# Kernel tuning notes

Measured on AMD Instinct MI355X. Metric: run time of the kernel, lower is better.

The kernel has to match this reference:

```python
import jax, jax.numpy as jnp
import numpy as np

D = 1024      # model dim
DH = 64       # dim_head
H = 8         # heads
INNER = DH * H
L = 6         # depth
NL = 64       # num_latents
MF = 128      # max_num_frames
FF = 4 * D    # ff_mult * dim
B, T, F, V = 4, 8, 4, 256


def _ln(x, g, b):
    m = x.mean(-1, keepdims=True)
    v = x.var(-1, keepdims=True)
    return (x - m) / jnp.sqrt(v + 1e-5) * g + b


def setup_inputs() -> dict:
    key = jax.random.key(0)
    ks = jax.random.split(key, 8)
    s = 0.02
    x = jax.random.normal(ks[0], (B, T, F, V, D), jnp.float32)
    latents = jax.random.normal(ks[1], (NL, D), jnp.float32)
    frame_embs = jax.random.normal(ks[2], (MF, D), jnp.float32)
    Wq = jax.random.normal(ks[3], (L, D, INNER), jnp.float32) * s
    Wkv = jax.random.normal(ks[4], (L, D, 2 * INNER), jnp.float32) * s
    Wo = jax.random.normal(ks[5], (L, INNER, D), jnp.float32) * s
    W1 = jax.random.normal(ks[6], (L, D, FF), jnp.float32) * s
    W2 = jax.random.normal(ks[7], (L, FF, D), jnp.float32) * s
    ones = jnp.ones((L, D), jnp.float32)
    zeros = jnp.zeros((L, D), jnp.float32)
    return dict(
        x=x, latents=latents, frame_embs=frame_embs,
        g_media=ones, b_media=zeros, g_lat=ones, b_lat=zeros,
        Wq=Wq, Wkv=Wkv, Wo=Wo, g_ff=ones, b_ff=zeros, W1=W1, W2=W2,
        g_out=jnp.ones((D,), jnp.float32), b_out=jnp.zeros((D,), jnp.float32),
    )


def reference(x, latents, frame_embs, g_media, b_media, g_lat, b_lat,
              Wq, Wkv, Wo, g_ff, b_ff, W1, W2, g_out, b_out):
    scale = DH ** -0.5
    # add frame embeddings (indexed by T, as in original code), merge F,v dims
    x = x + frame_embs[:T][None, :, None, None, :]
    x = x.reshape(B, T, F * V, D)
    lat0 = jnp.broadcast_to(latents, (B, T, NL, D))

    def split_heads(a):  # (b, t, n, h*d) -> (b, h, t, n, d)
        return a.reshape(B, T, -1, H, DH).transpose(0, 3, 1, 2, 4)

    def block(lat, p):
        gm, bm, gl, bl, wq, wkv, wo, gf, bf, w1, w2 = p
        xm = _ln(x, gm, bm)
        ln_l = _ln(lat, gl, bl)
        q = (ln_l @ wq) * scale
        kv = jnp.concatenate([xm, ln_l], axis=-2) @ wkv
        k, v = jnp.split(kv, 2, axis=-1)
        q, k, v = split_heads(q), split_heads(k), split_heads(v)
        sim = jnp.einsum('bhtid,bhtjd->bhtij', q, k)
        attn = jax.nn.softmax(sim, axis=-1)
        o = jnp.einsum('bhtij,bhtjd->bhtid', attn, v)
        o = o.transpose(0, 2, 3, 1, 4).reshape(B, T, NL, INNER)
        lat = o @ wo + lat
        ff = jax.nn.gelu(_ln(lat, gf, bf) @ w1, approximate=False) @ w2
        return lat + ff, None

    lat, _ = jax.lax.scan(block, lat0,
                          (g_media, b_media, g_lat, b_lat, Wq, Wkv, Wo,
                           g_ff, b_ff, W1, W2))
    return _ln(lat, g_out, b_out)
```

## Files before the change

### kernel.cpp

```cpp
#include <hip/hip_runtime.h>
#include <math.h>

#define D_      1024
#define DH_     64
#define H_      8
#define INNER_  512
#define L_      6
#define NL_     64
#define FF_     4096
#define B_      4
#define T_      8
#define FV_     1024
#define BT_     32
#define MROWS_  32768
#define NKV_    1088
#define KVROWS_ 34816
#define ZB_     256

typedef __bf16 bf16;
typedef __bf16 bf16x8 __attribute__((ext_vector_type(8)));
typedef __bf16 bf16x4 __attribute__((ext_vector_type(4)));
typedef float  f32x4  __attribute__((ext_vector_type(4)));

#define BARRIER() { asm volatile("" ::: "memory"); __builtin_amdgcn_s_barrier(); asm volatile("" ::: "memory"); }
// ... 47 lines not shown
                                                 float* __restrict__ lat) {
    int row = blockIdx.x;
    int i = row & 63;
    int c = threadIdx.x * 4;
    float4 v = *(const float4*)(latents + (size_t)i * D_ + c);
    *(float4*)(lat + (size_t)row * D_ + c) = v;
}

template<int OUTF>
__global__ __launch_bounds__(256) void ln_k(const float* __restrict__ in,
                                            const float* __restrict__ g,
                                            const float* __restrict__ b,
                                            void* __restrict__ out) {
    __shared__ float red[8];
    int row = blockIdx.x;
    const float* x = in + (size_t)row * D_;
    int tid = threadIdx.x, c = tid * 4;
    float4 v = *(const float4*)(x + c);
    float s = v.x + v.y + v.z + v.w;
    float ss = v.x * v.x + v.y * v.y + v.z * v.z + v.w * v.w;
    s = wred_sum(s); ss = wred_sum(ss);
    if ((tid & 63) == 0) { red[tid >> 6] = s; red[4 + (tid >> 6)] = ss; }
    __syncthreads();
    s = red[0] + red[1] + red[2] + red[3];
    ss = red[4] + red[5] + red[6] + red[7];
    float mean = s * (1.0f / D_);
    float rstd = rsqrtf(ss * (1.0f / D_) - mean * mean + 1e-5f);
    float4 gv = *(const float4*)(g + c);
    float4 bv = *(const float4*)(b + c);
    float o0 = (v.x - mean) * rstd * gv.x + bv.x;
    float o1 = (v.y - mean) * rstd * gv.y + bv.y;
    float o2 = (v.z - mean) * rstd * gv.z + bv.z;
    float o3 = (v.w - mean) * rstd * gv.w + bv.w;
    if (OUTF) {
        *(float4*)((float*)out + (size_t)row * D_ + c) = make_float4(o0, o1, o2, o3);
    } else {
        bf16x4 o; o[0] = (bf16)o0; o[1] = (bf16)o1; o[2] = (bf16)o2; o[3] = (bf16)o3;
        *(bf16x4*)((bf16*)out + (size_t)row * D_ + c) = o;
    }
}

template<int NP, int OUTF>
__global__ __launch_bounds__(256) void accln_k(float* __restrict__ lat,
                                               const float* __restrict__ p, long long s,
                                               const float* __restrict__ g,
                                               const float* __restrict__ b,
                                               void* __restrict__ out) {
    __shared__ float red[8];
    int row = blockIdx.x;
    int tid = threadIdx.x, c = tid * 4;
    float* lr = lat + (size_t)row * D_;
    float4 a = *(const float4*)(lr + c);
#pragma unroll
    for (int w = 0; w < NP; w++) {
        float4 x = *(const float4*)(p + (size_t)w * s + (size_t)row * D_ + c);
        a.x += x.x; a.y += x.y; a.z += x.z; a.w += x.w;
    }
    if (!OUTF) *(float4*)(lr + c) = a;
    float sm = a.x + a.y + a.z + a.w;
    float ss = a.x * a.x + a.y * a.y + a.z * a.z + a.w * a.w;
    sm = wred_sum(sm); ss = wred_sum(ss);
    if ((tid & 63) == 0) { red[tid >> 6] = sm; red[4 + (tid >> 6)] = ss; }
    __syncthreads();
    sm = red[0] + red[1] + red[2] + red[3];
    ss = red[4] + red[5] + red[6] + red[7];
    float mean = sm * (1.0f / D_);
    float rstd = rsqrtf(ss * (1.0f / D_) - mean * mean + 1e-5f);
    float4 gv = *(const float4*)(g + c);
    float4 bv = *(const float4*)(b + c);
    float o0 = (a.x - mean) * rstd * gv.x + bv.x;
    float o1 = (a.y - mean) * rstd * gv.y + bv.y;
    float o2 = (a.z - mean) * rstd * gv.z + bv.z;
    float o3 = (a.w - mean) * rstd * gv.w + bv.w;
    if (OUTF) {
        *(float4*)((float*)out + (size_t)row * D_ + c) = make_float4(o0, o1, o2, o3);
    } else {
        bf16x4 o; o[0] = (bf16)o0; o[1] = (bf16)o1; o[2] = (bf16)o2; o[3] = (bf16)o3;
        *(bf16x4*)((bf16*)out + (size_t)row * D_ + c) = o;
    }
}

__device__ __forceinline__ void wt_tile(const float* __restrict__ in, int R, int C,
                                        bf16* __restrict__ out, int bx, int by,
                                        const float* __restrict__ sc) {
    __shared__ float t[32][33];
    int c0 = bx * 32, r0 = by * 32;
    int tx = threadIdx.x & 31, ty = threadIdx.x >> 5;
#pragma unroll
    for (int i = 0; i < 4; i++)
        t[ty + i * 8][tx] = in[(size_t)(r0 + ty + i * 8) * C + c0 + tx];
    __syncthreads();
    float scale = sc ? sc[r0 + tx] : 1.0f;
#pragma unroll
    for (int i = 0; i < 4; i++)
        out[(size_t)(c0 + ty + i * 8) * R + r0 + tx] = (bf16)(t[tx][ty + i * 8] * scale);
}

__global__ __launch_bounds__(256) void wprep_k(const float* __restrict__ wq,
                                               const float* __restrict__ wkv,
                                               const float* __restrict__ wo,
                                               const float* __restrict__ w1,
                                               const float* __restrict__ w2,
                                               const float* __restrict__ gm,
                                               bf16* __restrict__ BcatQ,
                                               bf16* __restrict__ BcatKV,
                                               bf16* __restrict__ WkvTg,
                                               bf16* __restrict__ WoT,
                                               bf16* __restrict__ W1T,
                                               bf16* __restrict__ W2T) {
    int id = blockIdx.x;
    if (id < 512)            wt_tile(wq, D_, INNER_, BcatQ, id & 15, id >> 4, nullptr);
    else if (id < 1536)  { int i = id - 512;  wt_tile(wkv, D_, 2 * INNER_, BcatKV, i & 31, i >> 5, nullptr); }
    else if (id < 2560)  { int i = id - 1536; wt_tile(wkv, D_, 2 * INNER_, WkvTg, i & 31, i >> 5, gm); }
    else if (id < 3072)  { int i = id - 2560; wt_tile(wo, INNER_, D_, WoT, i & 31, i >> 5, nullptr); }
    else if (id < 7168)  { int i = id - 3072; wt_tile(w1, D_, FF_, W1T, i & 127, i >> 7, nullptr); }
    else                 { int i = id - 7168; wt_tile(w2, FF_, D_, W2T, i & 31, i >> 5, nullptr); }
}

__global__ __launch_bounds__(256) void bias_k(const float* __restrict__ bm,
                                              const float* __restrict__ wkv,
                                              float* __restrict__ bkv) {
    int n = blockIdx.x * 256 + threadIdx.x;
    float s = 0.0f;
    for (int k = 0; k < D_; k++) s += bm[k] * wkv[(size_t)k * (2 * INNER_) + n];
    bkv[n] = s;
}

__global__ __launch_bounds__(512, 1) void gemm_kv(const bf16* __restrict__ Ag,
                                                  const bf16* __restrict__ Bg,
                                                  bf16* __restrict__ KVb,
                                                  bf16* __restrict__ vt,
                                                  const float* __restrict__ bias) {
    __shared__ bf16 lds[2][32768];
    const int lda = D_, ldb = D_;
    const int tid = threadIdx.x;
    const int w = tid >> 6, lane = tid & 63;
    const int wm = w >> 2, wn = w & 3;
    const size_t m0 = (size_t)blockIdx.x * 256;
    const size_t n0 = (size_t)blockIdx.y * 256;
    const int nt = 16;

    const int p0 = (w * 2) * 64 + lane, p1 = p0 + 64;
    const int sr0 = p0 >> 3, sk0 = ((p0 & 7) ^ (sr0 & 7)) * 8;
    const int sr1 = p1 >> 3, sk1 = ((p1 & 7) ^ (sr1 & 7)) * 8;
    const int scw0 = (w * 2) * 512, scw1 = scw0 + 512;

    auto STAGE = [&](const bf16* g, int ld, size_t row0, int k0, bf16* bufb, int rb) {
        gload_lds16(g + (row0 + sr0) * (size_t)ld + k0 + sk0, bufb + rb + scw0);
        gload_lds16(g + (row0 + sr1) * (size_t)ld + k0 + sk1, bufb + rb + scw1);
    };

    const int fr = lane & 15;
    const int pK0 = (((lane >> 4)) ^ (fr & 7)) * 8;
    const int pK1 = ((4 + (lane >> 4)) ^ (fr & 7)) * 8;
    const size_t aoff = (size_t)(wm * 128 + fr) * 64;
    const size_t boff = 16384 + (size_t)(wn * 64 + fr) * 64;

    f32x4 acc[8][4];
#pragma unroll
    for (int i = 0; i < 8; i++)
#pragma unroll
        for (int j = 0; j < 4; j++)
#pragma unroll
            for (int r = 0; r < 4; r++) acc[i][j][r] = 0.0f;

    STAGE(Bg, ldb, n0,       0, lds[0], 16384);
    STAGE(Bg, ldb, n0 + 128, 0, lds[0], 24576);
    STAGE(Ag, lda, m0,       0, lds[0], 0);
    STAGE(Ag, lda, m0 + 128, 0, lds[0], 8192);
    STAGE(Bg, ldb, n0,       64, lds[1], 16384);
    STAGE(Bg, ldb, n0 + 128, 64, lds[1], 24576);
    STAGE(Ag, lda, m0,       64, lds[1], 0);
    asm volatile("s_waitcnt vmcnt(6)");
    BARRIER();

    for (int t = 0; t < nt; ++t) {
        const bf16* lb = lds[t & 1];
        bf16* lbw = lds[t & 1];
        bf16* lbn = lds[(t + 1) & 1];
        const int kt1 = (t + 1) << 6, kt2 = (t + 2) << 6;
        bf16x8 bfr[4][2];

        {
#pragma unroll
            for (int j = 0; j < 4; j++) {
                bfr[j][0] = *(const bf16x8*)(lb + boff + j * 1024 + pK0);
                bfr[j][1] = *(const bf16x8*)(lb + boff + j * 1024 + pK1);
            }
            bf16x8 a00 = *(const bf16x8*)(lb + aoff + 0 * 1024 + pK0);
            bf16x8 a01 = *(const bf16x8*)(lb + aoff + 0 * 1024 + pK1);
            bf16x8 a10 = *(const bf16x8*)(lb + aoff + 1 * 1024 + pK0);
            bf16x8 a11 = *(const bf16x8*)(lb + aoff + 1 * 1024 + pK1);
            if (t + 1 < nt) STAGE(Ag, lda, m0 + 128, kt1, lbn, 8192);
            BARRIER();
            asm volatile("s_waitcnt lgkmcnt(0)");
            __builtin_amdgcn_s_setprio(1);
#pragma unroll
            for (int j = 0; j < 4; j++) {
                acc[0][j] = __builtin_amdgcn_mfma_f32_16x16x32_bf16(a00, bfr[j][0], acc[0][j], 0, 0, 0);
                acc[0][j] = __builtin_amdgcn_mfma_f32_16x16x32_bf16(a01, bfr[j][1], acc[0][j], 0, 0, 0);
                acc[1][j] = __builtin_amdgcn_mfma_f32_16x16x32_bf16(a10, bfr[j][0], acc[1][j], 0, 0, 0);
                acc[1][j] = __builtin_amdgcn_mfma_f32_16x16x32_bf16(a11, bfr[j][1], acc[1][j], 0, 0, 0);
            }
            __builtin_amdgcn_s_setprio(0);
            BARRIER();
        }
        {
            bf16x8 a00 = *(const bf16x8*)(lb + aoff + 2 * 1024 + pK0);
            bf16x8 a01 = *(const bf16x8*)(lb + aoff + 2 * 1024 + pK1);
            bf16x8 a10 = *(const bf16x8*)(lb + aoff + 3 * 1024 + pK0);
            bf16x8 a11 = *(const bf16x8*)(lb + aoff + 3 * 1024 + pK1);
            if (t + 2 < nt) STAGE(Bg, ldb, n0, kt2, lbw, 16384);
            BARRIER();
            asm volatile("s_waitcnt lgkmcnt(0)");
            __builtin_amdgcn_s_setprio(1);
#pragma unroll
            for (int j = 0; j < 4; j++) {
                acc[2][j] = __builtin_amdgcn_mfma_f32_16x16x32_bf16(a00, bfr[j][0], acc[2][j], 0, 0, 0);
                acc[2][j] = __builtin_amdgcn_mfma_f32_16x16x32_bf16(a01, bfr[j][1], acc[2][j], 0, 0, 0);
                acc[3][j] = __builtin_amdgcn_mfma_f32_16x16x32_bf16(a10, bfr[j][0], acc[3][j], 0, 0, 0);
                acc[3][j] = __builtin_amdgcn_mfma_f32_16x16x32_bf16(a11, bfr[j][1], acc[3][j], 0, 0, 0);
            }
            __builtin_amdgcn_s_setprio(0);
            BARRIER();
        }
        {
            bf16x8 a00 = *(const bf16x8*)(lb + aoff + 4 * 1024 + pK0);
            bf16x8 a01 = *(const bf16x8*)(lb + aoff + 4 * 1024 + pK1);
            bf16x8 a10 = *(const bf16x8*)(lb + aoff + 5 * 1024 + pK0);
            bf16x8 a11 = *(const bf16x8*)(lb + aoff + 5 * 1024 + pK1);
            if (t + 2 < nt) STAGE(Bg, ldb, n0 + 128, kt2, lbw, 24576);
            BARRIER();
            asm volatile("s_waitcnt lgkmcnt(0)");
            __builtin_amdgcn_s_setprio(1);
#pragma unroll
            for (int j = 0; j < 4; j++) {
                acc[4][j] = __builtin_amdgcn_mfma_f32_16x16x32_bf16(a00, bfr[j][0], acc[4][j], 0, 0, 0);
                acc[4][j] = __builtin_amdgcn_mfma_f32_16x16x32_bf16(a01, bfr[j][1], acc[4][j], 0, 0, 0);
                acc[5][j] = __builtin_amdgcn_mfma_f32_16x16x32_bf16(a10, bfr[j][0], acc[5][j], 0, 0, 0);
                acc[5][j] = __builtin_amdgcn_mfma_f32_16x16x32_bf16(a11, bfr[j][1], acc[5][j], 0, 0, 0);
            }
            __builtin_amdgcn_s_setprio(0);
            BARRIER();
        }
        {
            bf16x8 a00 = *(const bf16x8*)(lb + aoff + 6 * 1024 + pK0);
            bf16x8 a01 = *(const bf16x8*)(lb + aoff + 6 * 1024 + pK1);
            bf16x8 a10 = *(const bf16x8*)(lb + aoff + 7 * 1024 + pK0);
            bf16x8 a11 = *(const bf16x8*)(lb + aoff + 7 * 1024 + pK1);
            if (t + 2 < nt) STAGE(Ag, lda, m0, kt2, lbw, 0);
            BARRIER();
            asm volatile("s_waitcnt lgkmcnt(0)");
            __builtin_amdgcn_s_setprio(1);
#pragma unroll
            for (int j = 0; j < 4; j++) {
                acc[6][j] = __builtin_amdgcn_mfma_f32_16x16x32_bf16(a00, bfr[j][0], acc[6][j], 0, 0, 0);
                acc[6][j] = __builtin_amdgcn_mfma_f32_16x16x32_bf16(a01, bfr[j][1], acc[6][j], 0, 0, 0);
                acc[7][j] = __builtin_amdgcn_mfma_f32_16x16x32_bf16(a10, bfr[j][0], acc[7][j], 0, 0, 0);
                acc[7][j] = __builtin_amdgcn_mfma_f32_16x16x32_bf16(a11, bfr[j][1], acc[7][j], 0, 0, 0);
            }
            __builtin_amdgcn_s_setprio(0);
            if (t < nt - 2)       { asm volatile("s_waitcnt vmcnt(6)"); }
            else if (t == nt - 2) { asm volatile("s_waitcnt vmcnt(0)"); }
            BARRIER();
        }
    }

    const int fq = (lane >> 4) * 4;
#pragma unroll
    for (int i = 0; i < 8; i++)
#pragma unroll
        for (int j = 0; j < 4; j++) {
            size_t cb = n0 + wn * 64 + j * 16 + fr;
            float bv = bias[cb];
            size_t mb = m0 + wm * 128 + i * 16 + fq;
            if (cb < 512) {
#pragma unroll
                for (int r = 0; r < 4; r++) {
                    size_t m = mb + r;
                    size_t rb = m + ((m >> 10) << 6);
                    KVb[rb * 512 + cb] = (bf16)(acc[i][j][r] + bv);
                }
            } else {
                int hh = ((int)cb - 512) >> 6, dh = ((int)cb - 512) & 63;
                size_t bt = mb >> 10, jl = mb & 1023;
                bf16x4 v4;
#pragma unroll
                for (int r = 0; r < 4; r++) v4[r] = (bf16)(acc[i][j][r] + bv);
                *(bf16x4*)(vt + ((bt * 8 + hh) * 64 + dh) * (size_t)NKV_ + jl) = v4;
            }
        }
}

template<int MODE, int CMAP>
__global__ __launch_bounds__(256) void gemm128(const bf16* __restrict__ A, int lda,
                                               const bf16* __restrict__ Bw, int ldb,
                                               void* __restrict__ C, int ldc,
                                               int K, float scale,
                                               long long czs, void* __restrict__ C2,
                                               void* __restrict__ C3) {
    __shared__ bf16 As[128 * 32];
    __shared__ bf16 Bs[128 * 32];
    const int tid = threadIdx.x;
    const int wave = tid >> 6;
    const int lane = tid & 63;
    const size_t m0 = (size_t)blockIdx.x * 128;
    const size_t n0 = (size_t)blockIdx.y * 128;
    const int wm = (wave >> 1) * 64;
    const int wn = (wave & 1) * 64;

    const int klen = K / gridDim.z;
    const int koff = blockIdx.z * klen;

    const int r0 = tid >> 2;
    const int c0 = ((tid & 3) ^ ((tid >> 3) & 3)) * 8;
    const bf16* ga0 = A + (m0 + r0) * lda + c0 + koff;
    const bf16* ga1 = A + (m0 + r0 + 64) * lda + c0 + koff;
    const bf16* gb0 = Bw + (n0 + r0) * ldb + c0 + koff;
    const bf16* gb1 = Bw + (n0 + r0 + 64) * ldb + c0 + koff;
    bf16* la0 = As + wave * 512;
    bf16* la1 = As + 2048 + wave * 512;
    bf16* lb0 = Bs + wave * 512;
    bf16* lb1 = Bs + 2048 + wave * 512;

    f32x4 acc[4][4];
#pragma unroll
    for (int i = 0; i < 4; i++)
#pragma unroll
        for (int j = 0; j < 4; j++)
#pragma unroll
            for (int r = 0; r < 4; r++) acc[i][j][r] = 0.0f;

    const int fr = lane & 15;
    const int q = lane >> 4;
    const int sw = (q ^ ((fr >> 1) & 3)) * 8;

    for (int kt = 0; kt < klen; kt += 32) {
        gload_lds16(ga0 + kt, la0);
        gload_lds16(ga1 + kt, la1);
        gload_lds16(gb0 + kt, lb0);
        gload_lds16(gb1 + kt, lb1);
        __syncthreads();
        bf16x8 af[4], bfv[4];
#pragma unroll
        for (int i = 0; i < 4; i++) {
            af[i]  = *(const bf16x8*)(As + (wm + i * 16 + fr) * 32 + sw);
            bfv[i] = *(const bf16x8*)(Bs + (wn + i * 16 + fr) * 32 + sw);
        }
#pragma unroll
        for (int i = 0; i < 4; i++)
#pragma unroll
            for (int j = 0; j < 4; j++)
                acc[i][j] = __builtin_amdgcn_mfma_f32_16x16x32_bf16(af[i], bfv[j], acc[i][j], 0, 0, 0);
        __syncthreads();
    }

    const int fq = (lane >> 4) * 4;
#pragma unroll
    for (int i = 0; i < 4; i++)
#pragma unroll
        for (int j = 0; j < 4; j++) {
            size_t cb = n0 + wn + j * 16 + fr;
            size_t mb = m0 + wm + i * 16 + fq;
            if (CMAP == 3) {
                if (cb < 512) {
#pragma unroll
                    for (int r = 0; r < 4; r++)
                        ((bf16*)C)[(mb + r) * 512 + cb] = (bf16)(acc[i][j][r] * scale);
                } else if (cb < 1024) {
#pragma unroll
                    for (int r = 0; r < 4; r++) {
                        size_t m = mb + r;
                        size_t rb = (m >> 6) * (size_t)NKV_ + 1024 + (m & 63);
                        ((bf16*)C2)[rb * 512 + (cb - 512)] = (bf16)acc[i][j][r];
                    }
                } else {
                    int hh = ((int)cb - 1024) >> 6, dh = ((int)cb - 1024) & 63;
                    size_t bt = mb >> 6, jl = 1024 + (mb & 63);
                    bf16x4 v4;
#pragma unroll
                    for (int r = 0; r < 4; r++) v4[r] = (bf16)acc[i][j][r];
                    *(bf16x4*)((bf16*)C3 + ((bt * 8 + hh) * 64 + dh) * (size_t)NKV_ + jl) = v4;
                }
            } else {
#pragma unroll
                for (int r = 0; r < 4; r++) {
                    float v = acc[i][j][r];
                    if (MODE == 4) {
                        ((float*)C + blockIdx.z * czs)[(mb + r) * ldc + cb] = v;
                    } else {
                        if (MODE == 3) v = gelu_f(v);
                        ((bf16*)C)[(mb + r) * ldc + cb] = (bf16)v;
                    }
                }
            }
        }
}

__global__ __launch_bounds__(256, 2) void attn_k(const bf16* __restrict__ qb,
                                                 const bf16* __restrict__ KVb,
                                                 const bf16* __restrict__ vt,
                                                 bf16* __restrict__ ob) {
    __shared__ float comb[4][64 * 66];
    __shared__ float sc[4][64];
    __shared__ float mw[4][64], lw[4][64];
    const int z = blockIdx.x, bt = z >> 3, h = z & 7;
    const int tid = threadIdx.x, w = tid >> 6, lane = tid & 63;
    const int fr = lane & 15, g = lane >> 4;
    const bf16* Qz = qb + (size_t)(bt * 64) * INNER_ + h * DH_;
    const bf16* Kz = KVb + (size_t)bt * NKV_ * 512 + h * DH_;
    const bf16* Vz = vt + (size_t)z * (DH_ * NKV_);
    bf16* Pw = (bf16*)(&comb[w][0]);

    bf16x8 qf[4][2];
#pragma unroll
    for (int nj = 0; nj < 4; nj++)
#pragma unroll
        for (int ks = 0; ks < 2; ks++)
            qf[nj][ks] = *(const bf16x8*)(Qz + (size_t)(fr + 16 * nj) * INNER_ + g * 8 + ks * 32);

    f32x4 acc_o[4][4];
#pragma unroll
    for (int i = 0; i < 4; i++)
#pragma unroll
        for (int j = 0; j < 4; j++)
#pragma unroll
            for (int r = 0; r < 4; r++) acc_o[i][j][r] = 0.0f;
    float m_reg[4] = {-INFINITY, -INFINITY, -INFINITY, -INFINITY};
    float l_reg[4] = {0.0f, 0.0f, 0.0f, 0.0f};

    const int nch = (w == 0) ? 5 : 4;
    for (int ci = 0; ci < nch; ci++) {
        const int kc0 = (w + ci * 4) * 64;
        f32x4 s[4][4];
#pragma unroll
        for (int i = 0; i < 4; i++)
#pragma unroll
            for (int j = 0; j < 4; j++)
#pragma unroll
                for (int r = 0; r < 4; r++) s[i][j][r] = 0.0f;
#pragma unroll
        for (int ks = 0; ks < 2; ks++) {
            bf16x8 kf[4];
#pragma unroll
            for (int mi = 0; mi < 4; mi++)
                kf[mi] = *(const bf16x8*)(Kz + (size_t)(kc0 + fr + 16 * mi) * 512 + g * 8 + ks * 32);
#pragma unroll
            for (int mi = 0; mi < 4; mi++)
#pragma unroll
                for (int nj = 0; nj < 4; nj++)
                    s[mi][nj] = __builtin_amdgcn_mfma_f32_16x16x32_bf16(kf[mi], qf[nj][ks], s[mi][nj], 0, 0, 0);
        }
        float pmax[4];
#pragma unroll
        for (int nj = 0; nj < 4; nj++) {
            float mx = s[0][nj][0];
#pragma unroll
            for (int mi = 0; mi < 4; mi++)
#pragma unroll
                for (int r = 0; r < 4; r++) mx = fmaxf(mx, s[mi][nj][r]);
            mx = fmaxf(mx, __shfl_xor(mx, 16, 64));
            mx = fmaxf(mx, __shfl_xor(mx, 32, 64));
            pmax[nj] = mx;
        }
        bool grew = (pmax[0] > m_reg[0]) || (pmax[1] > m_reg[1]) ||
                    (pmax[2] > m_reg[2]) || (pmax[3] > m_reg[3]);
        if (__any(grew ? 1 : 0)) {
            float so[4];
#pragma unroll
            for (int nj = 0; nj < 4; nj++) {
                float mn = fmaxf(m_reg[nj], pmax[nj]);
                so[nj] = __expf(m_reg[nj] - mn);
                m_reg[nj] = mn;
                l_reg[nj] *= so[nj];
            }
            if (g == 0) {
#pragma unroll
// ... 60 lines not shown
    for (int mi = 0; mi < 4; mi++)
#pragma unroll
        for (int jd = 0; jd < 4; jd++)
#pragma unroll
            for (int r = 0; r < 4; r++)
                comb[w][(16 * mi + 4 * g + r) * 66 + fr + 16 * jd] = acc_o[mi][jd][r];
    __syncthreads();
    {
        int q = tid >> 2, d0 = (tid & 3) * 16;
        float M = fmaxf(fmaxf(mw[0][q], mw[1][q]), fmaxf(mw[2][q], mw[3][q]));
        float al[4], l = 0.0f;
#pragma unroll
        for (int ww = 0; ww < 4; ww++) { al[ww] = __expf(mw[ww][q] - M); l += al[ww] * lw[ww][q]; }
        float inv = 1.0f / l;
        bf16 outv[16];
#pragma unroll
        for (int dd = 0; dd < 16; dd++) {
            float o = 0.0f;
#pragma unroll
            for (int ww = 0; ww < 4; ww++) o += comb[ww][q * 66 + d0 + dd] * al[ww];
            outv[dd] = (bf16)(o * inv);
        }
        bf16* dst = ob + (size_t)(bt * 64 + q) * INNER_ + h * 64 + d0;
        *(bf16x8*)dst = *(bf16x8*)outv;
        *(bf16x8*)(dst + 8) = *(bf16x8*)(outv + 8);
    }
}

extern "C" void kernel_launch(void* const* d_in, const int* in_sizes, int n_in,
                              void* d_out, int out_size, void* d_ws, size_t ws_size,
                              hipStream_t stream) {
    const float* x       = (const float*)d_in[0];
    const float* latents = (const float*)d_in[1];
    const float* fe      = (const float*)d_in[2];
    const float* g_media = (const float*)d_in[3];
    const float* b_media = (const float*)d_in[4];
    const float* g_lat   = (const float*)d_in[5];
    const float* b_lat   = (const float*)d_in[6];
    const float* Wq      = (const float*)d_in[7];
    const float* Wkv     = (const float*)d_in[8];
    const float* Wo      = (const float*)d_in[9];
    const float* g_ff    = (const float*)d_in[10];
    const float* b_ff    = (const float*)d_in[11];
    const float* W1      = (const float*)d_in[12];
    const float* W2      = (const float*)d_in[13];
    const float* g_out   = (const float*)d_in[14];
    const float* b_out   = (const float*)d_in[15];

    char* p = (char*)d_ws;
    auto alloc = [&](size_t bytes) { char* r = p; p += (bytes + 255) & ~(size_t)255; return r; };
    bf16*  xhat = (bf16*)alloc((size_t)MROWS_ * D_ * 2);
    float* lat  = (float*)alloc((size_t)2048 * D_ * 4);
    bf16*  lnl  = (bf16*)alloc((size_t)2048 * D_ * 2);
    bf16*  qb   = (bf16*)alloc((size_t)2048 * INNER_ * 2);
    bf16*  KVb  = (bf16*)alloc((size_t)KVROWS_ * 512 * 2);
    bf16*  vt   = (bf16*)alloc((size_t)ZB_ * DH_ * NKV_ * 2);
    bf16*  ob   = (bf16*)alloc((size_t)2048 * INNER_ * 2);
    bf16*  Bcat = (bf16*)alloc((size_t)1536 * D_ * 2);
    bf16*  WkvTg= (bf16*)alloc((size_t)D_ * D_ * 2);
    bf16*  WoT  = (bf16*)alloc((size_t)D_ * INNER_ * 2);
    bf16*  W1T  = (bf16*)alloc((size_t)FF_ * D_ * 2);
    bf16*  W2T  = (bf16*)alloc((size_t)D_ * FF_ * 2);
    float* bkv  = (float*)alloc(1024 * 4);
    float* ffp  = (float*)alloc((size_t)4 * 2048 * D_ * 4);
    bf16*  ffh  = vt;

    xhat_k<<<MROWS_, 256, 0, stream>>>(x, fe, xhat);
    latinit_k<<<2048, 256, 0, stream>>>(latents, lat);
    ln_k<0><<<2048, 256, 0, stream>>>(lat, g_lat, b_lat, lnl);

    const long long PS = (long long)2048 * D_;

    for (int l = 0; l < L_; l++) {
        const float* gm = g_media + (size_t)l * D_;
        const float* bm = b_media + (size_t)l * D_;
        const float* gf = g_ff + (size_t)l * D_;
        const float* bf_ = b_ff + (size_t)l * D_;
        const float* wq = Wq + (size_t)l * D_ * INNER_;
        const float* wkv = Wkv + (size_t)l * D_ * 2 * INNER_;
        const float* wo = Wo + (size_t)l * INNER_ * D_;
        const float* w1 = W1 + (size_t)l * D_ * FF_;
        const float* w2 = W2 + (size_t)l * FF_ * D_;

        wprep_k<<<11264, 256, 0, stream>>>(wq, wkv, wo, w1, w2, gm,
                                           Bcat, Bcat + (size_t)512 * D_, WkvTg, WoT, W1T, W2T);
        bias_k<<<4, 256, 0, stream>>>(bm, wkv, bkv);

        gemm_kv<<<dim3(128, 4), 512, 0, stream>>>(xhat, WkvTg, KVb, vt, bkv);
        gemm128<0, 3><<<dim3(16, 12), 256, 0, stream>>>(
            lnl, D_, Bcat, D_, qb, 0, D_, 0.125f, 0, KVb, vt);

        attn_k<<<ZB_, 256, 0, stream>>>(qb, KVb, vt, ob);

        gemm128<4, 0><<<dim3(16, 8, 2), 256, 0, stream>>>(
            ob, INNER_, WoT, INNER_, ffp, D_, INNER_, 1.0f, PS, nullptr, nullptr);
        accln_k<2, 0><<<2048, 256, 0, stream>>>(lat, ffp, PS, gf, bf_, lnl);

        gemm128<3, 0><<<dim3(16, 32), 256, 0, stream>>>(
            lnl, D_, W1T, D_, ffh, FF_, D_, 1.0f, 0, nullptr, nullptr);
        gemm128<4, 0><<<dim3(16, 8, 4), 256, 0, stream>>>(
            ffh, FF_, W2T, FF_, ffp, D_, FF_, 1.0f, PS, nullptr, nullptr);
        if (l < L_ - 1) {
            accln_k<4, 0><<<2048, 256, 0, stream>>>(lat, ffp, PS,
                g_lat + (size_t)(l + 1) * D_, b_lat + (size_t)(l + 1) * D_, lnl);
        } else {
            accln_k<4, 1><<<2048, 256, 0, stream>>>(lat, ffp, PS, g_out, b_out, (float*)d_out);
        }
    }
}
```

Baseline: 1.583 ms.

## Add pipelined 128x256 MFMA kernel for FF GEMMs and parallelize KV bias

Replaces the generic 128x128 gemm128 for the two feed-forward GEMMs with a new 512-thread gemm_ff kernel. It uses 128x256 tiles, a 64-wide K step, double-buffered direct-to-LDS loads, swizzled LDS and staged prefetch interleaved with MFMA phases, with GELU fused into the W1 epilogue. The KV bias reduction is also split across 32 K-chunks with atomicAdd after a memset, so it no longer runs on 4 blocks. The goal is more data reuse and overlap in the large FF GEMMs. The cost is fewer blocks per GEMM (256 and 256) on a large CU count, plus float atomics that make the bias sum order nondeterministic.

```diff
diff --git a/kernel.cpp b/kernel.cpp
--- a/kernel.cpp
+++ b/kernel.cpp
@@ -192,9 +192,11 @@
                                               const float* __restrict__ wkv,
                                               float* __restrict__ bkv) {
     int n = blockIdx.x * 256 + threadIdx.x;
+    int k0 = blockIdx.y * 32;
     float s = 0.0f;
-    for (int k = 0; k < D_; k++) s += bm[k] * wkv[(size_t)k * (2 * INNER_) + n];
-    bkv[n] = s;
+#pragma unroll
+    for (int k = k0; k < k0 + 32; k++) s += bm[k] * wkv[(size_t)k * (2 * INNER_) + n];
+    atomicAdd(&bkv[n], s);
 }
 
 __global__ __launch_bounds__(512, 1) void gemm_kv(const bf16* __restrict__ Ag,
@@ -359,6 +361,147 @@
 #pragma unroll
                 for (int r = 0; r < 4; r++) v4[r] = (bf16)(acc[i][j][r] + bv);
                 *(bf16x4*)(vt + ((bt * 8 + hh) * 64 + dh) * (size_t)NKV_ + jl) = v4;
+            }
+        }
+}
+
+template<int MODE>
+__global__ __launch_bounds__(512, 1) void gemm_ff(const bf16* __restrict__ Ag, int lda,
+                                                  const bf16* __restrict__ Bg, int ldb,
+                                                  void* __restrict__ C, int ldc,
+                                                  int K, long long czs) {
+    __shared__ bf16 lds[2][24576];
+    const int tid = threadIdx.x;
+    const int w = tid >> 6, lane = tid & 63;
+    const int wm = w >> 2, wn = w & 3;
+    const size_t m0 = (size_t)blockIdx.x * 128;
+    const size_t n0 = (size_t)blockIdx.y * 256;
+    const int klen = K / gridDim.z;
+    const int koff = blockIdx.z * klen;
+    const int nt = klen >> 6;
+
+    const int p0 = (w * 2) * 64 + lane, p1 = p0 + 64;
+    const int sr0 = p0 >> 3, sk0 = ((p0 & 7) ^ (sr0 & 7)) * 8;
+    const int sr1 = p1 >> 3, sk1 = ((p1 & 7) ^ (sr1 & 7)) * 8;
+    const int scw0 = (w * 2) * 512, scw1 = scw0 + 512;
+
+    auto STAGE = [&](const bf16* g, int ld, size_t row0, int k0, bf16* bufb, int rb) {
+        gload_lds16(g + (row0 + sr0) * (size_t)ld + k0 + sk0, bufb + rb + scw0);
+        gload_lds16(g + (row0 + sr1) * (size_t)ld + k0 + sk1, bufb + rb + scw1);
+    };
+
+    const int fr = lane & 15;
+    const int pK0 = (((lane >> 4)) ^ (fr & 7)) * 8;
+    const int pK1 = ((4 + (lane >> 4)) ^ (fr & 7)) * 8;
+    const size_t aoff = (size_t)(wm * 64 + fr) * 64;
+    const size_t boff = 8192 + (size_t)(wn * 64 + fr) * 64;
+
+    f32x4 acc[4][4];
+#pragma unroll
+    for (int i = 0; i < 4; i++)
+#pragma unroll
+        for (int j = 0; j < 4; j++)
+#pragma unroll
+            for (int r = 0; r < 4; r++) acc[i][j][r] = 0.0f;
+
+    STAGE(Ag, lda, m0,       koff,      lds[0], 0);
+    STAGE(Bg, ldb, n0,       koff,      lds[0], 8192);
+    STAGE(Bg, ldb, n0 + 128, koff,      lds[0], 16384);
+    STAGE(Bg, ldb, n0,       koff + 64, lds[1], 8192);
+    STAGE(Bg, ldb, n0 + 128, koff + 64, lds[1], 16384);
+    asm volatile("s_waitcnt vmcnt(4)");
+    BARRIER();
+
+    for (int t = 0; t < nt; ++t) {
+        const bf16* lb = lds[t & 1];
+        bf16* lbw = lds[t & 1];
+        bf16* lbn = lds[(t + 1) & 1];
+        const int kt1 = koff + ((t + 1) << 6), kt2 = koff + ((t + 2) << 6);
+        bf16x8 bfr[4][2];
+
+        {
+#pragma unroll
+            for (int j = 0; j < 4; j++) {
+                bfr[j][0] = *(const bf16x8*)(lb + boff + j * 1024 + pK0);
+                bfr[j][1] = *(const bf16x8*)(lb + boff + j * 1024 + pK1);
+            }
+            bf16x8 a0 = *(const bf16x8*)(lb + aoff + 0 * 1024 + pK0);
+            bf16x8 a1 = *(const bf16x8*)(lb + aoff + 0 * 1024 + pK1);
+            if (t + 1 < nt) STAGE(Ag, lda, m0, kt1, lbn, 0);
+            BARRIER();
+            asm volatile("s_waitcnt lgkmcnt(0)");
+            __builtin_amdgcn_s_setprio(1);
+#pragma unroll
+            for (int j = 0; j < 4; j++) {
+                acc[0][j] = __builtin_amdgcn_mfma_f32_16x16x32_bf16(a0, bfr[j][0], acc[0][j], 0, 0, 0);
+                acc[0][j] = __builtin_amdgcn_mfma_f32_16x16x32_bf16(a1, bfr[j][1], acc[0][j], 0, 0, 0);
+            }
+            __builtin_amdgcn_s_setprio(0);
+            BARRIER();
+        }
+        {
+            bf16x8 a0 = *(const bf16x8*)(lb + aoff + 1 * 1024 + pK0);
+            bf16x8 a1 = *(const bf16x8*)(lb + aoff + 1 * 1024 + pK1);
+            if (t + 2 < nt) STAGE(Bg, ldb, n0, kt2, lbw, 8192);
+            BARRIER();
+            asm volatile("s_waitcnt lgkmcnt(0)");
+            __builtin_amdgcn_s_setprio(1);
+#pragma unroll
+            for (int j = 0; j < 4; j++) {
+                acc[1][j] = __builtin_amdgcn_mfma_f32_16x16x32_bf16(a0, bfr[j][0], acc[1][j], 0, 0, 0);
+                acc[1][j] = __builtin_amdgcn_mfma_f32_16x16x32_bf16(a1, bfr[j][1], acc[1][j], 0, 0, 0);
+            }
+            __builtin_amdgcn_s_setprio(0);
+            BARRIER();
+        }
+        {
+            bf16x8 a0 = *(const bf16x8*)(lb + aoff + 2 * 1024 + pK0);
+            bf16x8 a1 = *(const bf16x8*)(lb + aoff + 2 * 1024 + pK1);
+            if (t + 2 < nt) STAGE(Bg, ldb, n0 + 128, kt2, lbw, 16384);
+            BARRIER();
+            asm volatile("s_waitcnt lgkmcnt(0)");
+            __builtin_amdgcn_s_setprio(1);
+#pragma unroll
+            for (int j = 0; j < 4; j++) {
+                acc[2][j] = __builtin_amdgcn_mfma_f32_16x16x32_bf16(a0, bfr[j][0], acc[2][j], 0, 0, 0);
+                acc[2][j] = __builtin_amdgcn_mfma_f32_16x16x32_bf16(a1, bfr[j][1], acc[2][j], 0, 0, 0);
+            }
+            __builtin_amdgcn_s_setprio(0);
+            BARRIER();
+        }
+        {
+            bf16x8 a0 = *(const bf16x8*)(lb + aoff + 3 * 1024 + pK0);
+            bf16x8 a1 = *(const bf16x8*)(lb + aoff + 3 * 1024 + pK1);
+            BARRIER();
+            asm volatile("s_waitcnt lgkmcnt(0)");
+            __builtin_amdgcn_s_setprio(1);
+#pragma unroll
+            for (int j = 0; j < 4; j++) {
+                acc[3][j] = __builtin_amdgcn_mfma_f32_16x16x32_bf16(a0, bfr[j][0], acc[3][j], 0, 0, 0);
+                acc[3][j] = __builtin_amdgcn_mfma_f32_16x16x32_bf16(a1, bfr[j][1], acc[3][j], 0, 0, 0);
+            }
+            __builtin_amdgcn_s_setprio(0);
+            if (t < nt - 2)       { asm volatile("s_waitcnt vmcnt(4)"); }
+            else if (t == nt - 2) { asm volatile("s_waitcnt vmcnt(0)"); }
+            BARRIER();
+        }
+    }
+
+    const int fq = (lane >> 4) * 4;
+#pragma unroll
+    for (int i = 0; i < 4; i++)
+#pragma unroll
+        for (int j = 0; j < 4; j++) {
+            size_t cb = n0 + wn * 64 + j * 16 + fr;
+            size_t mb = m0 + wm * 64 + i * 16 + fq;
+#pragma unroll
+            for (int r = 0; r < 4; r++) {
+                float v = acc[i][j][r];
+                if (MODE == 4) {
+                    ((float*)C + blockIdx.z * czs)[(mb + r) * (size_t)ldc + cb] = v;
+                } else {
+                    ((bf16*)C)[(mb + r) * (size_t)ldc + cb] = (bf16)gelu_f(v);
+                }
             }
         }
 }
@@ -460,7 +603,6 @@
                     if (MODE == 4) {
                         ((float*)C + blockIdx.z * czs)[(mb + r) * ldc + cb] = v;
                     } else {
-                        if (MODE == 3) v = gelu_f(v);
                         ((bf16*)C)[(mb + r) * ldc + cb] = (bf16)v;
                     }
                 }
@@ -692,7 +834,8 @@
 
         wprep_k<<<11264, 256, 0, stream>>>(wq, wkv, wo, w1, w2, gm,
                                            Bcat, Bcat + (size_t)512 * D_, WkvTg, WoT, W1T, W2T);
-        bias_k<<<4, 256, 0, stream>>>(bm, wkv, bkv);
+        hipMemsetAsync(bkv, 0, 1024 * 4, stream);
+        bias_k<<<dim3(4, 32), 256, 0, stream>>>(bm, wkv, bkv);
 
         gemm_kv<<<dim3(128, 4), 512, 0, stream>>>(xhat, WkvTg, KVb, vt, bkv);
         gemm128<0, 3><<<dim3(16, 12), 256, 0, stream>>>(
@@ -704,10 +847,10 @@
             ob, INNER_, WoT, INNER_, ffp, D_, INNER_, 1.0f, PS, nullptr, nullptr);
         accln_k<2, 0><<<2048, 256, 0, stream>>>(lat, ffp, PS, gf, bf_, lnl);
 
-        gemm128<3, 0><<<dim3(16, 32), 256, 0, stream>>>(
-            lnl, D_, W1T, D_, ffh, FF_, D_, 1.0f, 0, nullptr, nullptr);
-        gemm128<4, 0><<<dim3(16, 8, 4), 256, 0, stream>>>(
-            ffh, FF_, W2T, FF_, ffp, D_, FF_, 1.0f, PS, nullptr, nullptr);
+        gemm_ff<3><<<dim3(16, 16), 512, 0, stream>>>(
+            lnl, D_, W1T, D_, ffh, FF_, D_, 0);
+        gemm_ff<4><<<dim3(16, 4, 4), 512, 0, stream>>>(
+            ffh, FF_, W2T, FF_, ffp, D_, FF_, PS);
         if (l < L_ - 1) {
             accln_k<4, 0><<<2048, 256, 0, stream>>>(lat, ffp, PS,
                 g_lat + (size_t)(l + 1) * D_, b_lat + (size_t)(l + 1) * D_, lnl);
```

Result: faster. 1.323 ms (-16.4%).

## Replace KV and FF GEMMs with direct-B-register GEMM using 128x256 tiles

Applied to the files above, without the earlier changes.

Introduces a templated gemm_bd kernel that stages only A through LDS and loads B fragments straight from global memory into registers, double-buffered, on a 128x256 block tile. This replaces both the big KV projection GEMM (formerly 256x256 with LDS-staged B) and the Wo/W1/W2 GEMMs that used gemm128. The separate bias_k launch is folded into wprep_k through atomicAdd reductions, preceded by a memset. The aim is to cut LDS traffic and barriers and to raise block count. The cost is more global/L2 traffic for B, and the atomic reduction of bkv makes its summation order nondeterministic.

```diff
diff --git a/kernel.cpp b/kernel.cpp
--- a/kernel.cpp
+++ b/kernel.cpp
@@ -153,7 +153,9 @@
 
 __device__ __forceinline__ void wt_tile(const float* __restrict__ in, int R, int C,
                                         bf16* __restrict__ out, int bx, int by,
-                                        const float* __restrict__ sc) {
+                                        const float* __restrict__ sc,
+                                        const float* __restrict__ bm,
+                                        float* __restrict__ bkv) {
     __shared__ float t[32][33];
     int c0 = bx * 32, r0 = by * 32;
     int tx = threadIdx.x & 31, ty = threadIdx.x >> 5;
@@ -165,6 +167,12 @@
 #pragma unroll
     for (int i = 0; i < 4; i++)
         out[(size_t)(c0 + ty + i * 8) * R + r0 + tx] = (bf16)(t[tx][ty + i * 8] * scale);
+    if (bm && ty == 0) {
+        float s = 0.0f;
+#pragma unroll
+        for (int r = 0; r < 32; r++) s += bm[r0 + r] * t[r][tx];
+        atomicAdd(&bkv[c0 + tx], s);
+    }
 }
 
 __global__ __launch_bounds__(256) void wprep_k(const float* __restrict__ wq,
@@ -173,6 +181,8 @@
                                                const float* __restrict__ w1,
                                                const float* __restrict__ w2,
                                                const float* __restrict__ gm,
+                                               const float* __restrict__ bm,
+                                               float* __restrict__ bkv,
                                                bf16* __restrict__ BcatQ,
                                                bf16* __restrict__ BcatKV,
                                                bf16* __restrict__ WkvTg,
@@ -180,185 +190,134 @@
                                                bf16* __restrict__ W1T,
                                                bf16* __restrict__ W2T) {
     int id = blockIdx.x;
-    if (id < 512)            wt_tile(wq, D_, INNER_, BcatQ, id & 15, id >> 4, nullptr);
-    else if (id < 1536)  { int i = id - 512;  wt_tile(wkv, D_, 2 * INNER_, BcatKV, i & 31, i >> 5, nullptr); }
-    else if (id < 2560)  { int i = id - 1536; wt_tile(wkv, D_, 2 * INNER_, WkvTg, i & 31, i >> 5, gm); }
-    else if (id < 3072)  { int i = id - 2560; wt_tile(wo, INNER_, D_, WoT, i & 31, i >> 5, nullptr); }
-    else if (id < 7168)  { int i = id - 3072; wt_tile(w1, D_, FF_, W1T, i & 127, i >> 7, nullptr); }
-    else                 { int i = id - 7168; wt_tile(w2, FF_, D_, W2T, i & 31, i >> 5, nullptr); }
-}
-
-__global__ __launch_bounds__(256) void bias_k(const float* __restrict__ bm,
-                                              const float* __restrict__ wkv,
-                                              float* __restrict__ bkv) {
-    int n = blockIdx.x * 256 + threadIdx.x;
-    float s = 0.0f;
-    for (int k = 0; k < D_; k++) s += bm[k] * wkv[(size_t)k * (2 * INNER_) + n];
-    bkv[n] = s;
-}
-
-__global__ __launch_bounds__(512, 1) void gemm_kv(const bf16* __restrict__ Ag,
-                                                  const bf16* __restrict__ Bg,
-                                                  bf16* __restrict__ KVb,
-                                                  bf16* __restrict__ vt,
-                                                  const float* __restrict__ bias) {
-    __shared__ bf16 lds[2][32768];
-    const int lda = D_, ldb = D_;
+    if (id < 512)            wt_tile(wq, D_, INNER_, BcatQ, id & 15, id >> 4, nullptr, nullptr, nullptr);
+    else if (id < 1536)  { int i = id - 512;  wt_tile(wkv, D_, 2 * INNER_, BcatKV, i & 31, i >> 5, nullptr, nullptr, nullptr); }
+    else if (id < 2560)  { int i = id - 1536; wt_tile(wkv, D_, 2 * INNER_, WkvTg, i & 31, i >> 5, gm, bm, bkv); }
+    else if (id < 3072)  { int i = id - 2560; wt_tile(wo, INNER_, D_, WoT, i & 31, i >> 5, nullptr, nullptr, nullptr); }
+    else if (id < 7168)  { int i = id - 3072; wt_tile(w1, D_, FF_, W1T, i & 127, i >> 7, nullptr, nullptr, nullptr); }
+    else                 { int i = id - 7168; wt_tile(w2, FF_, D_, W2T, i & 31, i >> 5, nullptr, nullptr, nullptr); }
+}
+
+template<int MODE>
+__global__ __launch_bounds__(512, 1) void gemm_bd(const bf16* __restrict__ Ag, int lda,
+                                                  const bf16* __restrict__ Bg, int ldb,
+                                                  void* __restrict__ C, int ldc, int K,
+                                                  const float* __restrict__ bias,
+                                                  long long czs, void* __restrict__ C2) {
+    __shared__ bf16 alds[2][8192];
     const int tid = threadIdx.x;
     const int w = tid >> 6, lane = tid & 63;
     const int wm = w >> 2, wn = w & 3;
-    const size_t m0 = (size_t)blockIdx.x * 256;
+    const size_t m0 = (size_t)blockIdx.x * 128;
     const size_t n0 = (size_t)blockIdx.y * 256;
-    const int nt = 16;
-
-    const int p0 = (w * 2) * 64 + lane, p1 = p0 + 64;
-    const int sr0 = p0 >> 3, sk0 = ((p0 & 7) ^ (sr0 & 7)) * 8;
-    const int sr1 = p1 >> 3, sk1 = ((p1 & 7) ^ (sr1 & 7)) * 8;
-    const int scw0 = (w * 2) * 512, scw1 = scw0 + 512;
-
-    auto STAGE = [&](const bf16* g, int ld, size_t row0, int k0, bf16* bufb, int rb) {
-        gload_lds16(g + (row0 + sr0) * (size_t)ld + k0 + sk0, bufb + rb + scw0);
-        gload_lds16(g + (row0 + sr1) * (size_t)ld + k0 + sk1, bufb + rb + scw1);
+    const int klen = K / gridDim.z;
+    const int koff = blockIdx.z * klen;
+    const int nt = klen >> 6;
+    const int fr = lane & 15, g = lane >> 4;
+
+    const int p0 = tid, p1 = 512 + tid;
+    const int ar0 = p0 >> 3, ak0 = ((p0 & 7) ^ (ar0 & 7)) * 8;
+    const int ar1 = p1 >> 3, ak1 = ((p1 & 7) ^ (ar1 & 7)) * 8;
+    const bf16* gA0 = Ag + (m0 + ar0) * (size_t)lda + koff + ak0;
+    const bf16* gA1 = Ag + (m0 + ar1) * (size_t)lda + koff + ak1;
+    const int ld0 = w * 512;
+    const int ld1 = 4096 + w * 512;
+
+    const bf16* gB = Bg + (n0 + wn * 64 + fr) * (size_t)ldb + koff + g * 8;
+
+    const int pK0 = (g ^ (fr & 7)) * 8;
+    const int pK1 = ((4 + g) ^ (fr & 7)) * 8;
+    const size_t aoff = (size_t)(wm * 64 + fr) * 64;
+
+    f32x4 acc[4][4];
+#pragma unroll
+    for (int i = 0; i < 4; i++)
+#pragma unroll
+        for (int j = 0; j < 4; j++)
+#pragma unroll
+            for (int r = 0; r < 4; r++) acc[i][j][r] = 0.0f;
+
+    bf16x8 b0[4][2], b1[4][2];
+
+    auto STAGE_A = [&](int kt, int buf) {
+        gload_lds16(gA0 + kt, alds[buf] + ld0);
+        gload_lds16(gA1 + kt, alds[buf] + ld1);
     };
-
-    const int fr = lane & 15;
-    const int pK0 = (((lane >> 4)) ^ (fr & 7)) * 8;
-    const int pK1 = ((4 + (lane >> 4)) ^ (fr & 7)) * 8;
-    const size_t aoff = (size_t)(wm * 128 + fr) * 64;
-    const size_t boff = 16384 + (size_t)(wn * 64 + fr) * 64;
-
-    f32x4 acc[8][4];
-#pragma unroll
-    for (int i = 0; i < 8; i++)
+    auto LOADB = [&](int kt, bf16x8 (&bb)[4][2]) {
 #pragma unroll
         for (int j = 0; j < 4; j++)
 #pragma unroll
-            for (int r = 0; r < 4; r++) acc[i][j][r] = 0.0f;
-
-    STAGE(Bg, ldb, n0,       0, lds[0], 16384);
-    STAGE(Bg, ldb, n0 + 128, 0, lds[0], 24576);
-    STAGE(Ag, lda, m0,       0, lds[0], 0);
-    STAGE(Ag, lda, m0 + 128, 0, lds[0], 8192);
-    STAGE(Bg, ldb, n0,       64, lds[1], 16384);
-    STAGE(Bg, ldb, n0 + 128, 64, lds[1], 24576);
-    STAGE(Ag, lda, m0,       64, lds[1], 0);
-    asm volatile("s_waitcnt vmcnt(6)");
-    BARRIER();
-
-    for (int t = 0; t < nt; ++t) {
-        const bf16* lb = lds[t & 1];
-        bf16* lbw = lds[t & 1];
-        bf16* lbn = lds[(t + 1) & 1];
-        const int kt1 = (t + 1) << 6, kt2 = (t + 2) << 6;
-        bf16x8 bfr[4][2];
-
-        {
+            for (int ks = 0; ks < 2; ks++)
+                bb[j][ks] = *(const bf16x8*)(gB + (size_t)(16 * j) * ldb + kt + ks * 32);
+    };
+    auto TILE = [&](int t, int cur, bf16x8 (&bc)[4][2], bf16x8 (&bn)[4][2]) {
+        const int kt1 = (t + 1) << 6;
+        if (t + 1 < nt) {
+            LOADB(kt1, bn);
+            STAGE_A(kt1, cur ^ 1);
+            asm volatile("s_waitcnt vmcnt(10)");
+        } else {
+            asm volatile("s_waitcnt vmcnt(0)");
+        }
+        BARRIER();
+        const bf16* al = alds[cur];
+        bf16x8 ar[4][2];
+#pragma unroll
+        for (int i = 0; i < 4; i++) {
+            ar[i][0] = *(const bf16x8*)(al + aoff + i * 1024 + pK0);
+            ar[i][1] = *(const bf16x8*)(al + aoff + i * 1024 + pK1);
+        }
+        __builtin_amdgcn_s_setprio(1);
+#pragma unroll
+        for (int i = 0; i < 4; i++)
 #pragma unroll
             for (int j = 0; j < 4; j++) {
-                bfr[j][0] = *(const bf16x8*)(lb + boff + j * 1024 + pK0);
-                bfr[j][1] = *(const bf16x8*)(lb + boff + j * 1024 + pK1);
+                acc[i][j] = __builtin_amdgcn_mfma_f32_16x16x32_bf16(ar[i][0], bc[j][0], acc[i][j], 0, 0, 0);
+                acc[i][j] = __builtin_amdgcn_mfma_f32_16x16x32_bf16(ar[i][1], bc[j][1], acc[i][j], 0, 0, 0);
             }
-            bf16x8 a00 = *(const bf16x8*)(lb + aoff + 0 * 1024 + pK0);
-            bf16x8 a01 = *(const bf16x8*)(lb + aoff + 0 * 1024 + pK1);
-            bf16x8 a10 = *(const bf16x8*)(lb + aoff + 1 * 1024 + pK0);
-            bf16x8 a11 = *(const bf16x8*)(lb + aoff + 1 * 1024 + pK1);
-            if (t + 1 < nt) STAGE(Ag, lda, m0 + 128, kt1, lbn, 8192);
-            BARRIER();
-            asm volatile("s_waitcnt lgkmcnt(0)");
-            __builtin_amdgcn_s_setprio(1);
-#pragma unroll
-            for (int j = 0; j < 4; j++) {
-                acc[0][j] = __builtin_amdgcn_mfma_f32_16x16x32_bf16(a00, bfr[j][0], acc[0][j], 0, 0, 0);
-                acc[0][j] = __builtin_amdgcn_mfma_f32_16x16x32_bf16(a01, bfr[j][1], acc[0][j], 0, 0, 0);
-                acc[1][j] = __builtin_amdgcn_mfma_f32_16x16x32_bf16(a10, bfr[j][0], acc[1][j], 0, 0, 0);
-                acc[1][j] = __builtin_amdgcn_mfma_f32_16x16x32_bf16(a11, bfr[j][1], acc[1][j], 0, 0, 0);
-            }
-            __builtin_amdgcn_s_setprio(0);
-            BARRIER();
-        }
-        {
-            bf16x8 a00 = *(const bf16x8*)(lb + aoff + 2 * 1024 + pK0);
-            bf16x8 a01 = *(const bf16x8*)(lb + aoff + 2 * 1024 + pK1);
-            bf16x8 a10 = *(const bf16x8*)(lb + aoff + 3 * 1024 + pK0);
-            bf16x8 a11 = *(const bf16x8*)(lb + aoff + 3 * 1024 + pK1);
-            if (t + 2 < nt) STAGE(Bg, ldb, n0, kt2, lbw, 16384);
-            BARRIER();
-            asm volatile("s_waitcnt lgkmcnt(0)");
-            __builtin_amdgcn_s_setprio(1);
-#pragma unroll
-            for (int j = 0; j < 4; j++) {
-                acc[2][j] = __builtin_amdgcn_mfma_f32_16x16x32_bf16(a00, bfr[j][0], acc[2][j], 0, 0, 0);
-                acc[2][j] = __builtin_amdgcn_mfma_f32_16x16x32_bf16(a01, bfr[j][1], acc[2][j], 0, 0, 0);
-                acc[3][j] = __builtin_amdgcn_mfma_f32_16x16x32_bf16(a10, bfr[j][0], acc[3][j], 0, 0, 0);
-                acc[3][j] = __builtin_amdgcn_mfma_f32_16x16x32_bf16(a11, bfr[j][1], acc[3][j], 0, 0, 0);
-            }
-            __builtin_amdgcn_s_setprio(0);
-            BARRIER();
-        }
-        {
-            bf16x8 a00 = *(const bf16x8*)(lb + aoff + 4 * 1024 + pK0);
-            bf16x8 a01 = *(const bf16x8*)(lb + aoff + 4 * 1024 + pK1);
-            bf16x8 a10 = *(const bf16x8*)(lb + aoff + 5 * 1024 + pK0);
-            bf16x8 a11 = *(const bf16x8*)(lb + aoff + 5 * 1024 + pK1);
-            if (t + 2 < nt) STAGE(Bg, ldb, n0 + 128, kt2, lbw, 24576);
-            BARRIER();
-            asm volatile("s_waitcnt lgkmcnt(0)");
-            __builtin_amdgcn_s_setprio(1);
-#pragma unroll
-            for (int j = 0; j < 4; j++) {
-                acc[4][j] = __builtin_amdgcn_mfma_f32_16x16x32_bf16(a00, bfr[j][0], acc[4][j], 0, 0, 0);
-                acc[4][j] = __builtin_amdgcn_mfma_f32_16x16x32_bf16(a01, bfr[j][1], acc[4][j], 0, 0, 0);
-                acc[5][j] = __builtin_amdgcn_mfma_f32_16x16x32_bf16(a10, bfr[j][0], acc[5][j], 0, 0, 0);
-                acc[5][j] = __builtin_amdgcn_mfma_f32_16x16x32_bf16(a11, bfr[j][1], acc[5][j], 0, 0, 0);
-            }
-            __builtin_amdgcn_s_setprio(0);
-            BARRIER();
-        }
-        {
-            bf16x8 a00 = *(const bf16x8*)(lb + aoff + 6 * 1024 + pK0);
-            bf16x8 a01 = *(const bf16x8*)(lb + aoff + 6 * 1024 + pK1);
-            bf16x8 a10 = *(const bf16x8*)(lb + aoff + 7 * 1024 + pK0);
-            bf16x8 a11 = *(const bf16x8*)(lb + aoff + 7 * 1024 + pK1);
-            if (t + 2 < nt) STAGE(Ag, lda, m0, kt2, lbw, 0);
-            BARRIER();
-            asm volatile("s_waitcnt lgkmcnt(0)");
-            __builtin_amdgcn_s_setprio(1);
-#pragma unroll
-            for (int j = 0; j < 4; j++) {
-                acc[6][j] = __builtin_amdgcn_mfma_f32_16x16x32_bf16(a00, bfr[j][0], acc[6][j], 0, 0, 0);
-                acc[6][j] = __builtin_amdgcn_mfma_f32_16x16x32_bf16(a01, bfr[j][1], acc[6][j], 0, 0, 0);
-                acc[7][j] = __builtin_amdgcn_mfma_f32_16x16x32_bf16(a10, bfr[j][0], acc[7][j], 0, 0, 0);
-                acc[7][j] = __builtin_amdgcn_mfma_f32_16x16x32_bf16(a11, bfr[j][1], acc[7][j], 0, 0, 0);
-            }
-            __builtin_amdgcn_s_setprio(0);
-            if (t < nt - 2)       { asm volatile("s_waitcnt vmcnt(6)"); }
-            else if (t == nt - 2) { asm volatile("s_waitcnt vmcnt(0)"); }
-            BARRIER();
-        }
-    }
-
-    const int fq = (lane >> 4) * 4;
-#pragma unroll
-    for (int i = 0; i < 8; i++)
+        __builtin_amdgcn_s_setprio(0);
+        BARRIER();
+    };
+
+    LOADB(0, b0);
+    STAGE_A(0, 0);
+    for (int t = 0; t < nt; t += 2) {
+        TILE(t, 0, b0, b1);
+        TILE(t + 1, 1, b1, b0);
+    }
+
+    const int fq = g * 4;
+#pragma unroll
+    for (int i = 0; i < 4; i++)
 #pragma unroll
         for (int j = 0; j < 4; j++) {
             size_t cb = n0 + wn * 64 + j * 16 + fr;
-            float bv = bias[cb];
-            size_t mb = m0 + wm * 128 + i * 16 + fq;
-            if (cb < 512) {
-#pragma unroll
-                for (int r = 0; r < 4; r++) {
-                    size_t m = mb + r;
-                    size_t rb = m + ((m >> 10) << 6);
-                    KVb[rb * 512 + cb] = (bf16)(acc[i][j][r] + bv);
+            size_t mb = m0 + wm * 64 + i * 16 + fq;
+            if (MODE == 0) {
+                float bv = bias[cb];
+                if (cb < 512) {
+#pragma unroll
+                    for (int r = 0; r < 4; r++) {
+                        size_t m = mb + r;
+                        size_t rb = m + ((m >> 10) << 6);
+                        ((bf16*)C)[rb * 512 + cb] = (bf16)(acc[i][j][r] + bv);
+                    }
+                } else {
+                    int hh = ((int)cb - 512) >> 6, dh = ((int)cb - 512) & 63;
+                    size_t bt = mb >> 10, jl = mb & 1023;
+                    bf16x4 v4;
+#pragma unroll
+                    for (int r = 0; r < 4; r++) v4[r] = (bf16)(acc[i][j][r] + bv);
+                    *(bf16x4*)((bf16*)C2 + ((bt * 8 + hh) * 64 + dh) * (size_t)NKV_ + jl) = v4;
                 }
+            } else if (MODE == 4) {
+#pragma unroll
+                for (int r = 0; r < 4; r++)
+                    ((float*)C + blockIdx.z * czs)[(mb + r) * (size_t)ldc + cb] = acc[i][j][r];
             } else {
-                int hh = ((int)cb - 512) >> 6, dh = ((int)cb - 512) & 63;
-                size_t bt = mb >> 10, jl = mb & 1023;
-                bf16x4 v4;
-#pragma unroll
-                for (int r = 0; r < 4; r++) v4[r] = (bf16)(acc[i][j][r] + bv);
-                *(bf16x4*)(vt + ((bt * 8 + hh) * 64 + dh) * (size_t)NKV_ + jl) = v4;
+#pragma unroll
+                for (int r = 0; r < 4; r++)
+                    ((bf16*)C)[(mb + r) * (size_t)ldc + cb] = (bf16)gelu_f(acc[i][j][r]);
             }
         }
 }
@@ -455,15 +414,8 @@
                 }
             } else {
 #pragma unroll
-                for (int r = 0; r < 4; r++) {
-                    float v = acc[i][j][r];
-                    if (MODE == 4) {
-                        ((float*)C + blockIdx.z * czs)[(mb + r) * ldc + cb] = v;
-                    } else {
-                        if (MODE == 3) v = gelu_f(v);
-                        ((bf16*)C)[(mb + r) * ldc + cb] = (bf16)v;
-                    }
-                }
+                for (int r = 0; r < 4; r++)
+                    ((bf16*)C)[(mb + r) * ldc + cb] = (bf16)acc[i][j][r];
             }
         }
 }
@@ -690,24 +642,25 @@
         const float* w1 = W1 + (size_t)l * D_ * FF_;
         const float* w2 = W2 + (size_t)l * FF_ * D_;
 
-        wprep_k<<<11264, 256, 0, stream>>>(wq, wkv, wo, w1, w2, gm,
+        hipMemsetAsync(bkv, 0, 1024 * 4, stream);
+        wprep_k<<<11264, 256, 0, stream>>>(wq, wkv, wo, w1, w2, gm, bm, bkv,
                                            Bcat, Bcat + (size_t)512 * D_, WkvTg, WoT, W1T, W2T);
-        bias_k<<<4, 256, 0, stream>>>(bm, wkv, bkv);
-
-        gemm_kv<<<dim3(128, 4), 512, 0, stream>>>(xhat, WkvTg, KVb, vt, bkv);
+
+        gemm_bd<0><<<dim3(256, 4), 512, 0, stream>>>(
+            xhat, D_, WkvTg, D_, KVb, 0, D_, bkv, 0, vt);
         gemm128<0, 3><<<dim3(16, 12), 256, 0, stream>>>(
             lnl, D_, Bcat, D_, qb, 0, D_, 0.125f, 0, KVb, vt);
 
         attn_k<<<ZB_, 256, 0, stream>>>(qb, KVb, vt, ob);
 
-        gemm128<4, 0><<<dim3(16, 8, 2), 256, 0, stream>>>(
-            ob, INNER_, WoT, INNER_, ffp, D_, INNER_, 1.0f, PS, nullptr, nullptr);
+        gemm_bd<4><<<dim3(16, 4, 2), 512, 0, stream>>>(
+            ob, INNER_, WoT, INNER_, ffp, D_, INNER_, nullptr, PS, nullptr);
         accln_k<2, 0><<<2048, 256, 0, stream>>>(lat, ffp, PS, gf, bf_, lnl);
 
-        gemm128<3, 0><<<dim3(16, 32), 256, 0, stream>>>(
-            lnl, D_, W1T, D_, ffh, FF_, D_, 1.0f, 0, nullptr, nullptr);
-        gemm128<4, 0><<<dim3(16, 8, 4), 256, 0, stream>>>(
-            ffh, FF_, W2T, FF_, ffp, D_, FF_, 1.0f, PS, nullptr, nullptr);
+        gemm_bd<3><<<dim3(16, 16), 512, 0, stream>>>(
+            lnl, D_, W1T, D_, ffh, FF_, D_, nullptr, 0, nullptr);
+        gemm_bd<4><<<dim3(16, 4, 4), 512, 0, stream>>>(
+            ffh, FF_, W2T, FF_, ffp, D_, FF_, nullptr, PS, nullptr);
         if (l < L_ - 1) {
             accln_k<4, 0><<<2048, 256, 0, stream>>>(lat, ffp, PS,
                 g_lat + (size_t)(l + 1) * D_, b_lat + (size_t)(l + 1) * D_, lnl);
```

After: 2.071 ms. 30.8% more time.
